# Optimization experiments

Measured on AMD Instinct MI355X. Metric: run time of the kernel, lower is better.

The kernel has to match this reference:

```python
import jax, jax.numpy as jnp
import numpy as np

TOP_K_FRACTION = 0.1


def setup_inputs() -> dict:
    key = jax.random.key(0)
    k1, k2, k3 = jax.random.split(key, 3)
    B, H, S, D = 2, 12, 1024, 64
    q = jax.random.normal(k1, (B, H, S, D), dtype=jnp.float32)
    k = jax.random.normal(k2, (B, H, S, D), dtype=jnp.float32)
    v = jax.random.normal(k3, (B, H, S, D), dtype=jnp.float32)
    mask = jnp.zeros((B, 1, 1, S), dtype=jnp.float32)
    return {"q": q, "k": k, "v": v, "mask": mask}


def reference(q, k, v, mask):
    B, H, S, D = q.shape
    k_precise = max(1, int(S * TOP_K_FRACTION))
    # binary (sign) approximation of attention scores; detached like torch
    q_bin = jnp.sign(jax.lax.stop_gradient(q))
    k_bin = jnp.sign(jax.lax.stop_gradient(k))
    approx_scores = jnp.einsum('bhsd,bhtd->bhst', q_bin, k_bin) / D  # [B,H,S,S]
    _, topk_idx = jax.lax.top_k(approx_scores, k_precise)  # [B,H,S,kp]
    # gather top-k keys/values per query: [B,H,S,kp,D]
    k_gathered = jnp.take_along_axis(k[:, :, None, :, :], topk_idx[..., None], axis=3)
    v_gathered = jnp.take_along_axis(v[:, :, None, :, :], topk_idx[..., None], axis=3)
    scale = np.float32(1.0 / np.sqrt(D))
    precise_scores = jnp.einsum('bhsd,bhskd->bhsk', q, k_gathered) * scale
    # gather mask along key positions: mask [B,1,1,S] -> [B,H,S,kp]
    mask_gathered = jnp.take_along_axis(
        jnp.broadcast_to(mask, (B, H, S, S)), topk_idx, axis=-1)
    precise_scores = precise_scores + mask_gathered
    precise_probs = jax.nn.softmax(precise_scores, axis=-1)
    attn_output = jnp.einsum('bhsk,bhskd->bhsd', precise_probs, v_gathered)
    return attn_output
```

## Files before the change

kernel.cpp:

```cpp
#include <hip/hip_runtime.h>
#include <hip/hip_fp16.h>
#include <cstdint>

#define BB 2
#define HH 12
#define SS 1024
#define DD 64
#define KP 102
#define KPAD 104
#define QPB 4

typedef _Float16 half2v __attribute__((ext_vector_type(2)));
typedef _Float16 half8v __attribute__((ext_vector_type(8)));

template <int CTRL>
__device__ __forceinline__ float dpp_f(float x) {
    return __builtin_bit_cast(float,
        __builtin_amdgcn_update_dpp(0, __builtin_bit_cast(int, x), CTRL, 0xF, 0xF, false));
}
__device__ __forceinline__ float readlane_f(float x, int l) {
    return __builtin_bit_cast(float,
        __builtin_amdgcn_readlane(__builtin_bit_cast(int, x), l));
}
__device__ __forceinline__ int bperm_i(int addr4, int src) {
    return __builtin_amdgcn_ds_bpermute(addr4, src);
}
__device__ __forceinline__ float bperm_f(int addr4, float src) {
    return __builtin_bit_cast(float,
        __builtin_amdgcn_ds_bpermute(addr4, __builtin_bit_cast(int, src)));
}
__device__ __forceinline__ float group8_sum(float x) {
    x += dpp_f<0xB1>(x);
    x += dpp_f<0x4E>(x);
    x += dpp_f<0x141>(x);
    return x;
}
__device__ __forceinline__ float wave_sum_f32(float x) {
    x += dpp_f<0xB1>(x);
    x += dpp_f<0x4E>(x);
    x += dpp_f<0x141>(x);
    x += dpp_f<0x140>(x);
    return (readlane_f(x, 0) + readlane_f(x, 16))
         + (readlane_f(x, 32) + readlane_f(x, 48));
}

__global__ __launch_bounds__(256) void pack_kernel(
    const float* __restrict__ k, const float* __restrict__ v,
    unsigned long long* __restrict__ kbits,
    _Float16* __restrict__ kh, _Float16* __restrict__ vh)
{
    int row  = (int)((blockIdx.x * 256 + threadIdx.x) >> 6);
    int lane = (int)(threadIdx.x & 63);
    if (row >= BB * HH * SS) return;
    float kv = k[(size_t)row * DD + lane];
    float vv = v[(size_t)row * DD + lane];
    unsigned long long km = __ballot(kv > 0.0f);
    kh[(size_t)row * DD + lane] = (_Float16)kv;
    vh[(size_t)row * DD + lane] = (_Float16)vv;
    if (lane == 0) kbits[row] = km;
}

__global__ __launch_bounds__(256, 4) void battn_kernel(
    const float* __restrict__ q, const _Float16* __restrict__ kh,
    const _Float16* __restrict__ vh, const float* __restrict__ mask,
    const unsigned long long* __restrict__ kbits,
    float* __restrict__ out)
{
    const int tid  = (int)threadIdx.x;
    const int w    = tid >> 6;
    const int lane = tid & 63;
    const int query = (int)blockIdx.x * QPB + w;
    const int bh    = query >> 10;
    const int b     = bh / HH;

    __shared__ int   sel_t[QPB][KPAD];
    __shared__ float sel_p[QPB][KPAD];

    const float qreg = q[(size_t)query * DD + lane];
    const unsigned long long qm = __ballot(qreg > 0.0f);

    const unsigned long long* kb = kbits + (size_t)bh * SS;
    int pbin[16];
    #pragma unroll
    for (int j = 0; j < 16; ++j)
        pbin[j] = (int)__popcll(qm ^ kb[j * 64 + lane]);

    #define COUNT_LE(P, OUTC)                                      \
        { int _c = 0;                                              \
          _Pragma("unroll")                                        \
          for (int j = 0; j < 16; ++j)                             \
              _c += (int)__popcll(__ballot(pbin[j] <= (P)));       \
          (OUTC) = _c; }
    int P = 27, c, clt;
    COUNT_LE(P, c);
    if (c >= KP) {
        COUNT_LE(P - 1, clt);
        while (clt >= KP) {
            c = clt; --P;
            COUNT_LE(P - 1, clt);
        }
    } else {
        do { clt = c; ++P; COUNT_LE(P, c); } while (c < KP);
    }
    const int binP = P;
    const int need = KP - clt;
    #undef COUNT_LE

    const unsigned long long lmask_lt = (lane == 0) ? 0ULL : (~0ULL >> (64 - lane));
    int base = 0, tie_base = 0;
    #pragma unroll
    for (int j = 0; j < 16; ++j) {
        bool isGt  = pbin[j] < binP;
        bool isTie = (pbin[j] == binP);
        unsigned long long tiem = __ballot(isTie);
        int rank = tie_base + (int)__popcll(tiem & lmask_lt);
        bool take = isGt || (isTie && rank < need);
        unsigned long long tm = __ballot(take);
        if (take)
            sel_t[w][base + (int)__popcll(tm & lmask_lt)] = j * 64 + lane;
        base     += (int)__popcll(tm);
        tie_base += (int)__popcll(tiem);
    }

    const int t0 = sel_t[w][lane];
    const int t1 = (lane < KP - 64) ? sel_t[w][lane + 64] : 0;

    const int sub = lane & 7, g = lane >> 3;
    const float* qrow = q + (size_t)query * DD + sub * 8;
    half2v qh[4];
    #pragma unroll
    for (int d = 0; d < 4; ++d) {
        float2 f2 = *(const float2*)(qrow + d * 2);
        half2v h; h[0] = (_Float16)(f2.x * 0.125f); h[1] = (_Float16)(f2.y * 0.125f);
        qh[d] = h;
    }
    const _Float16* krows = kh + (size_t)bh * SS * DD;
    int treg[13];
    #pragma unroll
    for (int ii = 0; ii < 13; ++ii) {
        const int i0 = ii * 8;
        const int addr = ((i0 & 63) + g) << 2;
        int t = bperm_i(addr, (i0 < 64) ? t0 : t1);
        treg[ii] = t;
        half8v kv8 = *(const half8v*)(krows + (size_t)t * DD + sub * 8);
        half2v k0; k0[0] = kv8[0]; k0[1] = kv8[1];
        half2v k1; k1[0] = kv8[2]; k1[1] = kv8[3];
        half2v k2; k2[0] = kv8[4]; k2[1] = kv8[5];
        half2v k3; k3[0] = kv8[6]; k3[1] = kv8[7];
        float partial = __builtin_amdgcn_fdot2(qh[0], k0, 0.0f, false);
        partial = __builtin_amdgcn_fdot2(qh[1], k1, partial, false);
        partial = __builtin_amdgcn_fdot2(qh[2], k2, partial, false);
        partial = __builtin_amdgcn_fdot2(qh[3], k3, partial, false);
        partial = group8_sum(partial);
        if (sub == 0) sel_p[w][i0 + g] = partial;
    }

    const float* maskrow = mask + (size_t)b * SS;
    const bool has2 = (lane < KP - 64);
    float p0 = sel_p[w][lane] + maskrow[t0];
    float e0 = __expf(p0);
    float e1 = 0.0f;
    if (has2) e1 = __expf(sel_p[w][lane + 64] + maskrow[t1]);
    float rinv = __frcp_rn(wave_sum_f32(e0 + e1));
    float w0 = e0 * rinv;
    float w1 = e1 * rinv;

    const _Float16* vrows = vh + (size_t)bh * SS * DD;
    float acc[8] = {0.f, 0.f, 0.f, 0.f, 0.f, 0.f, 0.f, 0.f};
    #pragma unroll
    for (int ii = 0; ii < 13; ++ii) {
        const int i0 = ii * 8;
        const int addr = ((i0 & 63) + g) << 2;
        float wt = bperm_f(addr, (i0 < 64) ? w0 : w1);
        half8v vv = *(const half8v*)(vrows + (size_t)treg[ii] * DD + sub * 8);
        #pragma unroll
        for (int d = 0; d < 8; ++d)
            acc[d] = fmaf(wt, (float)vv[d], acc[d]);
    }
    #pragma unroll
    for (int d = 0; d < 8; ++d) {
        float x = acc[d];
        x += __shfl_xor(x, 8);
        x += __shfl_xor(x, 16);
        x += __shfl_xor(x, 32);
        acc[d] = x;
    }
    if (lane < 8) {
        float* orow = out + (size_t)query * DD + lane * 8;
        float4 o0 = make_float4(acc[0], acc[1], acc[2], acc[3]);
        float4 o1 = make_float4(acc[4], acc[5], acc[6], acc[7]);
        *(float4*)orow       = o0;
        *(float4*)(orow + 4) = o1;
    }
}

extern "C" void kernel_launch(void* const* d_in, const int* in_sizes, int n_in,
                              void* d_out, int out_size, void* d_ws, size_t ws_size,
                              hipStream_t stream) {
    const float* q    = (const float*)d_in[0];
    const float* k    = (const float*)d_in[1];
    const float* v    = (const float*)d_in[2];
    const float* mask = (const float*)d_in[3];
    float* out = (float*)d_out;

    const int rows = BB * HH * SS;
    unsigned long long* kbits = (unsigned long long*)d_ws;
    _Float16* kh = (_Float16*)((char*)d_ws + (size_t)rows * sizeof(unsigned long long));
    _Float16* vh = kh + (size_t)rows * DD;

    pack_kernel<<<(rows * 64 + 255) / 256, 256, 0, stream>>>(k, v, kbits, kh, vh);
    battn_kernel<<<rows / QPB, 256, 0, stream>>>(q, kh, vh, mask, kbits, out);
}
```

Measured before the change: 120.8 us.

## Fuse score, exp and PV accumulation into single pass with fp16 accumulators

Merges the separate score, softmax and value-gather loops into one loop that loads K and V rows together, exponentiates each score with a fixed offset instead of a max, and accumulates weighted V in packed fp16. The normalization sum is reduced once at the end and applied to the output. This removes the shared-memory score buffer, the bpermute shuffles and the second gather pass, and overlaps the K and V loads. The risks are reduced precision from fp16 accumulation and possible overflow if scores exceed the fixed offset's assumed range.

```diff
diff --git a/kernel.cpp b/kernel.cpp
--- a/kernel.cpp
+++ b/kernel.cpp
@@ -18,30 +18,11 @@
     return __builtin_bit_cast(float,
         __builtin_amdgcn_update_dpp(0, __builtin_bit_cast(int, x), CTRL, 0xF, 0xF, false));
 }
-__device__ __forceinline__ float readlane_f(float x, int l) {
-    return __builtin_bit_cast(float,
-        __builtin_amdgcn_readlane(__builtin_bit_cast(int, x), l));
-}
-__device__ __forceinline__ int bperm_i(int addr4, int src) {
-    return __builtin_amdgcn_ds_bpermute(addr4, src);
-}
-__device__ __forceinline__ float bperm_f(int addr4, float src) {
-    return __builtin_bit_cast(float,
-        __builtin_amdgcn_ds_bpermute(addr4, __builtin_bit_cast(int, src)));
-}
 __device__ __forceinline__ float group8_sum(float x) {
     x += dpp_f<0xB1>(x);
     x += dpp_f<0x4E>(x);
     x += dpp_f<0x141>(x);
     return x;
-}
-__device__ __forceinline__ float wave_sum_f32(float x) {
-    x += dpp_f<0xB1>(x);
-    x += dpp_f<0x4E>(x);
-    x += dpp_f<0x141>(x);
-    x += dpp_f<0x140>(x);
-    return (readlane_f(x, 0) + readlane_f(x, 16))
-         + (readlane_f(x, 32) + readlane_f(x, 48));
 }
 
 __global__ __launch_bounds__(256) void pack_kernel(
@@ -73,8 +54,7 @@
     const int bh    = query >> 10;
     const int b     = bh / HH;
 
-    __shared__ int   sel_t[QPB][KPAD];
-    __shared__ float sel_p[QPB][KPAD];
+    __shared__ int sel_t[QPB][KPAD];
 
     const float qreg = q[(size_t)query * DD + lane];
     const unsigned long long qm = __ballot(qreg > 0.0f);
@@ -95,10 +75,7 @@
     COUNT_LE(P, c);
     if (c >= KP) {
         COUNT_LE(P - 1, clt);
-        while (clt >= KP) {
-            c = clt; --P;
-            COUNT_LE(P - 1, clt);
-        }
+        while (clt >= KP) { c = clt; --P; COUNT_LE(P - 1, clt); }
     } else {
         do { clt = c; ++P; COUNT_LE(P, c); } while (c < KP);
     }
@@ -107,6 +84,8 @@
     #undef COUNT_LE
 
     const unsigned long long lmask_lt = (lane == 0) ? 0ULL : (~0ULL >> (64 - lane));
+    if (lane < KPAD - KP)
+        sel_t[w][KP + lane] = 0;
     int base = 0, tie_base = 0;
     #pragma unroll
     for (int j = 0; j < 16; ++j) {
@@ -122,9 +101,6 @@
         tie_base += (int)__popcll(tiem);
     }
 
-    const int t0 = sel_t[w][lane];
-    const int t1 = (lane < KP - 64) ? sel_t[w][lane + 64] : 0;
-
     const int sub = lane & 7, g = lane >> 3;
     const float* qrow = q + (size_t)query * DD + sub * 8;
     half2v qh[4];
@@ -134,49 +110,54 @@
         half2v h; h[0] = (_Float16)(f2.x * 0.125f); h[1] = (_Float16)(f2.y * 0.125f);
         qh[d] = h;
     }
-    const _Float16* krows = kh + (size_t)bh * SS * DD;
-    int treg[13];
+    const _Float16* krows   = kh + (size_t)bh * SS * DD;
+    const _Float16* vrows   = vh + (size_t)bh * SS * DD;
+    const float*    maskrow = mask + (size_t)b * SS;
+
+    half2v acch[4];
+    #pragma unroll
+    for (int d = 0; d < 4; ++d) { acch[d][0] = (_Float16)0; acch[d][1] = (_Float16)0; }
+    float l_part = 0.0f;
+
     #pragma unroll
     for (int ii = 0; ii < 13; ++ii) {
-        const int i0 = ii * 8;
-        const int addr = ((i0 & 63) + g) << 2;
-        int t = bperm_i(addr, (i0 < 64) ? t0 : t1);
-        treg[ii] = t;
-        half8v kv8 = *(const half8v*)(krows + (size_t)t * DD + sub * 8);
+        const int i = ii * 8 + g;
+        const int t = sel_t[w][i];
+        const _Float16* kp = krows + (size_t)t * DD + sub * 8;
+        const _Float16* vp = vrows + (size_t)t * DD + sub * 8;
+        half8v kv8 = *(const half8v*)kp;
+        half8v vv8 = *(const half8v*)vp;
         half2v k0; k0[0] = kv8[0]; k0[1] = kv8[1];
         half2v k1; k1[0] = kv8[2]; k1[1] = kv8[3];
         half2v k2; k2[0] = kv8[4]; k2[1] = kv8[5];
         half2v k3; k3[0] = kv8[6]; k3[1] = kv8[7];
-        float partial = __builtin_amdgcn_fdot2(qh[0], k0, 0.0f, false);
-        partial = __builtin_amdgcn_fdot2(qh[1], k1, partial, false);
-        partial = __builtin_amdgcn_fdot2(qh[2], k2, partial, false);
-        partial = __builtin_amdgcn_fdot2(qh[3], k3, partial, false);
-        partial = group8_sum(partial);
-        if (sub == 0) sel_p[w][i0 + g] = partial;
+        float s = __builtin_amdgcn_fdot2(qh[0], k0, 0.0f, false);
+        s = __builtin_amdgcn_fdot2(qh[1], k1, s, false);
+        s = __builtin_amdgcn_fdot2(qh[2], k2, s, false);
+        s = __builtin_amdgcn_fdot2(qh[3], k3, s, false);
+        s = group8_sum(s);
+        float e = __expf(s + maskrow[t] - 4.0f);
+        if (ii == 12 && i >= KP) e = 0.0f;
+        l_part += e;
+        _Float16 eh = (_Float16)e;
+        half2v e2; e2[0] = eh; e2[1] = eh;
+        #pragma unroll
+        for (int d = 0; d < 4; ++d) {
+            half2v v2; v2[0] = vv8[d * 2]; v2[1] = vv8[d * 2 + 1];
+            acch[d] = e2 * v2 + acch[d];
+        }
     }
 
-    const float* maskrow = mask + (size_t)b * SS;
-    const bool has2 = (lane < KP - 64);
-    float p0 = sel_p[w][lane] + maskrow[t0];
-    float e0 = __expf(p0);
-    float e1 = 0.0f;
-    if (has2) e1 = __expf(sel_p[w][lane + 64] + maskrow[t1]);
-    float rinv = __frcp_rn(wave_sum_f32(e0 + e1));
-    float w0 = e0 * rinv;
-    float w1 = e1 * rinv;
-
-    const _Float16* vrows = vh + (size_t)bh * SS * DD;
-    float acc[8] = {0.f, 0.f, 0.f, 0.f, 0.f, 0.f, 0.f, 0.f};
+    float acc[8];
     #pragma unroll
-    for (int ii = 0; ii < 13; ++ii) {
-        const int i0 = ii * 8;
-        const int addr = ((i0 & 63) + g) << 2;
-        float wt = bperm_f(addr, (i0 < 64) ? w0 : w1);
-        half8v vv = *(const half8v*)(vrows + (size_t)treg[ii] * DD + sub * 8);
-        #pragma unroll
-        for (int d = 0; d < 8; ++d)
-            acc[d] = fmaf(wt, (float)vv[d], acc[d]);
+    for (int d = 0; d < 4; ++d) {
+        acc[d * 2]     = (float)acch[d][0];
+        acc[d * 2 + 1] = (float)acch[d][1];
     }
+    float l = l_part;
+    l += __shfl_xor(l, 8);
+    l += __shfl_xor(l, 16);
+    l += __shfl_xor(l, 32);
     #pragma unroll
     for (int d = 0; d < 8; ++d) {
         float x = acc[d];
@@ -185,10 +166,13 @@
         x += __shfl_xor(x, 32);
         acc[d] = x;
     }
+    const float rinv = __frcp_rn(l);
     if (lane < 8) {
         float* orow = out + (size_t)query * DD + lane * 8;
-        float4 o0 = make_float4(acc[0], acc[1], acc[2], acc[3]);
-        float4 o1 = make_float4(acc[4], acc[5], acc[6], acc[7]);
+        float4 o0 = make_float4(acc[0] * rinv, acc[1] * rinv,
+                                acc[2] * rinv, acc[3] * rinv);
+        float4 o1 = make_float4(acc[4] * rinv, acc[5] * rinv,
+                                acc[6] * rinv, acc[7] * rinv);
         *(float4*)orow       = o0;
         *(float4*)(orow + 4) = o1;
     }
```

New measurement: 111.3 us. 1.09x faster.
